# Kernel tuning notes

Hardware: AMD Instinct MI355X
Metric: run time of the kernel (lower is better)

The kernel has to match this reference:

```python
import jax, jax.numpy as jnp
import numpy as np

B, C, H, D, HID = 1024, 64, 64, 256, 256

def setup_inputs() -> dict:
    key = jax.random.key(0)
    k1, k2, k3, k4, k5, k6, k7, k8 = jax.random.split(key, 8)
    candidate_news_vector = jax.random.normal(k1, (B, C, D), dtype=jnp.float32)
    clicked_news_vector = jax.random.normal(k2, (B, H, D), dtype=jnp.float32)
    mask_cand = jax.random.randint(k3, (B, C), 0, 2).astype(bool).at[:, 0].set(True)
    mask_hist = jax.random.randint(k4, (B, H), 0, 2).astype(bool).at[:, 0].set(True)
    # nn.Linear default init: U(-1/sqrt(fan_in), 1/sqrt(fan_in))
    s1 = 1.0 / np.sqrt(2 * D)
    s2 = 1.0 / np.sqrt(HID)
    W1 = jax.random.uniform(k5, (HID, 2 * D), minval=-s1, maxval=s1, dtype=jnp.float32)
    b1 = jax.random.uniform(k6, (HID,), minval=-s1, maxval=s1, dtype=jnp.float32)
    W2 = jax.random.uniform(k7, (1, HID), minval=-s2, maxval=s2, dtype=jnp.float32)
    b2 = jax.random.uniform(k8, (1,), minval=-s2, maxval=s2, dtype=jnp.float32)
    return {"candidate_news_vector": candidate_news_vector,
            "clicked_news_vector": clicked_news_vector,
            "mask_cand": mask_cand, "mask_hist": mask_hist,
            "W1": W1, "b1": b1, "W2": W2, "b2": b2}

def reference(candidate_news_vector, clicked_news_vector, mask_cand, mask_hist, W1, b1, W2, b2):
    d = candidate_news_vector.shape[-1]
    w2 = W2[0]                                  # [HID]
    # Two stacked Linears with no nonlinearity collapse exactly:
    # score = (W2 @ W1_c) . cand + (W2 @ W1_h) . hist + (W2 @ b1 + b2)
    v_c = W1[:, :d].T @ w2                      # [D]
    v_h = W1[:, d:].T @ w2                      # [D]
    bias = jnp.dot(w2, b1) + b2[0]
    scores = (jnp.einsum('bcd,d->bc', candidate_news_vector, v_c)[:, :, None]
              + jnp.einsum('bhd,d->bh', clicked_news_vector, v_h)[:, None, :]
              + bias)                           # [B, C, H]
    neg = jnp.finfo(scores.dtype).min
    scores = jnp.where(mask_hist[:, None, :], scores, neg)
    weights = jax.nn.softmax(scores, axis=-1)   # [B, C, H]
    weights = jnp.where(mask_cand[:, :, None], weights, 0.0)
    user_vector = jnp.einsum('bch,bhd->bcd', weights, clicked_news_vector)
    return user_vector
```

## Files before the change

kernel.cpp:

```cpp
#include <hip/hip_runtime.h>
#include <math.h>

#define NB 1024
#define NC 64
#define NH 64
#define ND 256
#define NHID 256

__device__ __forceinline__ bool read_mask(const void* m, int idx, int mode) {
  if (mode == 2) return ((const float*)m)[idx] != 0.0f;
  if (mode == 1) return ((const unsigned char*)m)[idx] != 0;
  return ((const int*)m)[idx] != 0;
}

__global__ __launch_bounds__(1024) void precompute_kernel(
    const float* __restrict__ W1, const float* __restrict__ W2,
    const unsigned int* __restrict__ mask_cand,
    const unsigned int* __restrict__ mask_hist,
    float* __restrict__ ws)
{
  __shared__ float w2_lds[NHID];
  __shared__ float partial[4][ND];
  int t = threadIdx.x;
  if (t < NHID) w2_lds[t] = W2[t];
  __syncthreads();
  int d = t & (ND - 1);
  int g = t >> 8;
  float acc = 0.f;
  #pragma unroll 8
  for (int j = g * 64; j < g * 64 + 64; ++j)
    acc = fmaf(W1[(size_t)j * (2 * ND) + ND + d], w2_lds[j], acc);
  partial[g][d] = acc;
  __syncthreads();
  if (t < ND)
    ws[t] = partial[0][t] + partial[1][t] + partial[2][t] + partial[3][t];
  if (t == 0) {
    int sawf = 0; unsigned int big = 0;
    for (int i = 0; i < 32; ++i) {
      unsigned int a = mask_hist[i], b = mask_cand[i];
      if (a == 0x3f800000u || b == 0x3f800000u) sawf = 1;
      if ((a > 1u && a != 0x3f800000u) || (b > 1u && b != 0x3f800000u)) big = 1;
    }
    ((int*)ws)[ND] = sawf ? 2 : (big ? 1 : 0);
  }
}

__global__ __launch_bounds__(256) void user_encoder_kernel(
    const float* __restrict__ hist,
    const void* __restrict__ mask_cand_v,
    const void* __restrict__ mask_hist_v,
    const float* __restrict__ ws,
    float* __restrict__ out)
{
  const int b = blockIdx.x;
  const int t = threadIdx.x;
  const int wave = t >> 6;
  const int lane = t & 63;

  __shared__ float s_lds[NH];
  __shared__ float w_lds[NH];
  __shared__ float4 part[4][64];
  __shared__ float4 uv_lds[64];

  const int mode = ((const int*)ws)[ND];
  const float* hb = hist + (size_t)b * NH * ND;

  float4 xs[16];
  #pragma unroll
  for (int hh = 0; hh < 16; ++hh)
    xs[hh] = reinterpret_cast<const float4*>(hb + (size_t)(wave * 16 + hh) * ND)[lane];

  const float4 vh4 = reinterpret_cast<const float4*>(ws)[lane];
  #pragma unroll
  for (int hh = 0; hh < 16; ++hh) {
    float4 x = xs[hh];
    float p = fmaf(x.x, vh4.x, fmaf(x.y, vh4.y, fmaf(x.z, vh4.z, x.w * vh4.w)));
    #pragma unroll
    for (int off = 32; off; off >>= 1) p += __shfl_xor(p, off);
    if (lane == 0) {
      int h = wave * 16 + hh;
      bool mh = read_mask(mask_hist_v, b * NH + h, mode);
      s_lds[h] = mh ? p : -3.0e38f;
    }
  }
  __syncthreads();

  if (wave == 0) {
    float s = s_lds[lane];
    float m = s;
    #pragma unroll
    for (int off = 32; off; off >>= 1) m = fmaxf(m, __shfl_xor(m, off));
    float e = expf(s - m);
    float sum = e;
    #pragma unroll
    for (int off = 32; off; off >>= 1) sum += __shfl_xor(sum, off);
    w_lds[lane] = e / sum;
  }
  __syncthreads();

  float4 acc = {0.f, 0.f, 0.f, 0.f};
  #pragma unroll
  for (int hh = 0; hh < 16; ++hh) {
    float wgt = w_lds[wave * 16 + hh];
    float4 x = xs[hh];
    acc.x = fmaf(wgt, x.x, acc.x);
    acc.y = fmaf(wgt, x.y, acc.y);
    acc.z = fmaf(wgt, x.z, acc.z);
    acc.w = fmaf(wgt, x.w, acc.w);
  }
  part[wave][lane] = acc;
  __syncthreads();
  if (t < 64) {
    float4 a = part[0][t], b4 = part[1][t], c4 = part[2][t], d4 = part[3][t];
    float4 s4;
    s4.x = a.x + b4.x + c4.x + d4.x;
    s4.y = a.y + b4.y + c4.y + d4.y;
    s4.z = a.z + b4.z + c4.z + d4.z;
    s4.w = a.w + b4.w + c4.w + d4.w;
    uv_lds[t] = s4;
  }
  __syncthreads();

  float4* ob = reinterpret_cast<float4*>(out + (size_t)b * NC * ND);
  const float4 val = uv_lds[lane];
  const float4 zero = {0.f, 0.f, 0.f, 0.f};
  #pragma unroll
  for (int k = 0; k < 16; ++k) {
    int c = k * 4 + wave;
    bool mc = read_mask(mask_cand_v, b * NC + c, mode);
    ob[k * 256 + t] = mc ? val : zero;
  }
}

extern "C" void kernel_launch(void* const* d_in, const int* in_sizes, int n_in,
                              void* d_out, int out_size, void* d_ws, size_t ws_size,
                              hipStream_t stream) {
  (void)in_sizes; (void)n_in; (void)out_size; (void)ws_size;
  const float* hist = (const float*)d_in[1];
  const void*  mask_cand = d_in[2];
  const void*  mask_hist = d_in[3];
  const float* W1 = (const float*)d_in[4];
  const float* W2 = (const float*)d_in[6];
  float* ws = (float*)d_ws;
  float* out = (float*)d_out;

  precompute_kernel<<<1, 1024, 0, stream>>>(
      W1, W2, (const unsigned int*)mask_cand, (const unsigned int*)mask_hist, ws);
  user_encoder_kernel<<<NB, 256, 0, stream>>>(hist, mask_cand, mask_hist, ws, out);
}
```

Baseline: 45.45 us.

## Parallelize W1 reduction across blocks and widen main kernel to 512 threads

```diff
diff --git a/kernel.cpp b/kernel.cpp
--- a/kernel.cpp
+++ b/kernel.cpp
@@ -7,13 +7,57 @@
 #define ND 256
 #define NHID 256
 
+typedef float f4 __attribute__((ext_vector_type(4)));
+
+#define WS_PART_OFF 1024
+
 __device__ __forceinline__ bool read_mask(const void* m, int idx, int mode) {
   if (mode == 2) return ((const float*)m)[idx] != 0.0f;
   if (mode == 1) return ((const unsigned char*)m)[idx] != 0;
   return ((const int*)m)[idx] != 0;
 }
 
-__global__ __launch_bounds__(1024) void precompute_kernel(
+__device__ __forceinline__ void detect_mode(const unsigned int* mask_cand,
+                                            const unsigned int* mask_hist,
+                                            int* dst) {
+  int sawf = 0; unsigned int big = 0;
+  for (int i = 0; i < 32; ++i) {
+    unsigned int a = mask_hist[i], b = mask_cand[i];
+    if (a == 0x3f800000u || b == 0x3f800000u) sawf = 1;
+    if ((a > 1u && a != 0x3f800000u) || (b > 1u && b != 0x3f800000u)) big = 1;
+  }
+  *dst = sawf ? 2 : (big ? 1 : 0);
+}
+
+__global__ __launch_bounds__(256) void precompute_p1(
+    const float* __restrict__ W1, const float* __restrict__ W2,
+    float* __restrict__ ws)
+{
+  const int g = blockIdx.x;
+  const int d = threadIdx.x;
+  float acc = 0.f;
+  #pragma unroll
+  for (int jj = 0; jj < 4; ++jj) {
+    int j = g * 4 + jj;
+    acc = fmaf(W1[(size_t)j * (2 * ND) + ND + d], W2[j], acc);
+  }
+  ws[WS_PART_OFF + g * ND + d] = acc;
+}
+
+__global__ __launch_bounds__(256) void precompute_p2(
+    const unsigned int* __restrict__ mask_cand,
+    const unsigned int* __restrict__ mask_hist,
+    float* __restrict__ ws)
+{
+  const int d = threadIdx.x;
+  float acc = 0.f;
+  #pragma unroll 8
+  for (int g = 0; g < 64; ++g) acc += ws[WS_PART_OFF + g * ND + d];
+  ws[d] = acc;
+  if (d == 0) detect_mode(mask_cand, mask_hist, (int*)ws + ND);
+}
+
+__global__ __launch_bounds__(1024) void precompute_fallback(
     const float* __restrict__ W1, const float* __restrict__ W2,
     const unsigned int* __restrict__ mask_cand,
     const unsigned int* __restrict__ mask_hist,
@@ -34,18 +78,10 @@
   __syncthreads();
   if (t < ND)
     ws[t] = partial[0][t] + partial[1][t] + partial[2][t] + partial[3][t];
-  if (t == 0) {
-    int sawf = 0; unsigned int big = 0;
-    for (int i = 0; i < 32; ++i) {
-      unsigned int a = mask_hist[i], b = mask_cand[i];
-      if (a == 0x3f800000u || b == 0x3f800000u) sawf = 1;
-      if ((a > 1u && a != 0x3f800000u) || (b > 1u && b != 0x3f800000u)) big = 1;
-    }
-    ((int*)ws)[ND] = sawf ? 2 : (big ? 1 : 0);
-  }
+  if (t == 0) detect_mode(mask_cand, mask_hist, (int*)ws + ND);
 }
 
-__global__ __launch_bounds__(256) void user_encoder_kernel(
+__global__ __launch_bounds__(512, 8) void user_encoder_kernel(
     const float* __restrict__ hist,
     const void* __restrict__ mask_cand_v,
     const void* __restrict__ mask_hist_v,
@@ -54,38 +90,33 @@
 {
   const int b = blockIdx.x;
   const int t = threadIdx.x;
-  const int wave = t >> 6;
   const int lane = t & 63;
+  const int w = t >> 6;
 
   __shared__ float s_lds[NH];
-  __shared__ float w_lds[NH];
-  __shared__ float4 part[4][64];
-  __shared__ float4 uv_lds[64];
+  __shared__ float4 part[8][64];
 
   const int mode = ((const int*)ws)[ND];
-  const float* hb = hist + (size_t)b * NH * ND;
+  const float4* hb4 = reinterpret_cast<const float4*>(hist + (size_t)b * NH * ND);
+  const float4* vh4p = reinterpret_cast<const float4*>(ws);
 
-  float4 xs[16];
-  #pragma unroll
-  for (int hh = 0; hh < 16; ++hh)
-    xs[hh] = reinterpret_cast<const float4*>(hb + (size_t)(wave * 16 + hh) * ND)[lane];
-
-  const float4 vh4 = reinterpret_cast<const float4*>(ws)[lane];
-  #pragma unroll
-  for (int hh = 0; hh < 16; ++hh) {
-    float4 x = xs[hh];
-    float p = fmaf(x.x, vh4.x, fmaf(x.y, vh4.y, fmaf(x.z, vh4.z, x.w * vh4.w)));
+  {
+    const int r = t >> 3, cg = t & 7;
+    float p = 0.f;
     #pragma unroll
-    for (int off = 32; off; off >>= 1) p += __shfl_xor(p, off);
-    if (lane == 0) {
-      int h = wave * 16 + hh;
-      bool mh = read_mask(mask_hist_v, b * NH + h, mode);
-      s_lds[h] = mh ? p : -3.0e38f;
+    for (int i = 0; i < 8; ++i) {
+      float4 x = hb4[r * 64 + i * 8 + cg];
+      float4 v = vh4p[i * 8 + cg];
+      p = fmaf(x.x, v.x, fmaf(x.y, v.y, fmaf(x.z, v.z, fmaf(x.w, v.w, p))));
     }
+    p += __shfl_xor(p, 1); p += __shfl_xor(p, 2); p += __shfl_xor(p, 4);
+    if (cg == 0)
+      s_lds[r] = read_mask(mask_hist_v, b * NH + r, mode) ? p : -3.0e38f;
   }
   __syncthreads();
 
-  if (wave == 0) {
+  float wval;
+  {
     float s = s_lds[lane];
     float m = s;
     #pragma unroll
@@ -94,48 +125,46 @@
     float sum = e;
     #pragma unroll
     for (int off = 32; off; off >>= 1) sum += __shfl_xor(sum, off);
-    w_lds[lane] = e / sum;
+    wval = e / sum;
+  }
+
+  {
+    float4 acc = {0.f, 0.f, 0.f, 0.f};
+    #pragma unroll
+    for (int j = 0; j < 8; ++j) {
+      float wj = __shfl(wval, (w << 3) | j);
+      float4 x = hb4[((w << 3) | j) * 64 + lane];
+      acc.x = fmaf(wj, x.x, acc.x);
+      acc.y = fmaf(wj, x.y, acc.y);
+      acc.z = fmaf(wj, x.z, acc.z);
+      acc.w = fmaf(wj, x.w, acc.w);
+    }
+    part[w][lane] = acc;
   }
   __syncthreads();
 
-  float4 acc = {0.f, 0.f, 0.f, 0.f};
-  #pragma unroll
-  for (int hh = 0; hh < 16; ++hh) {
-    float wgt = w_lds[wave * 16 + hh];
-    float4 x = xs[hh];
-    acc.x = fmaf(wgt, x.x, acc.x);
-    acc.y = fmaf(wgt, x.y, acc.y);
-    acc.z = fmaf(wgt, x.z, acc.z);
-    acc.w = fmaf(wgt, x.w, acc.w);
-  }
-  part[wave][lane] = acc;
-  __syncthreads();
-  if (t < 64) {
-    float4 a = part[0][t], b4 = part[1][t], c4 = part[2][t], d4 = part[3][t];
-    float4 s4;
-    s4.x = a.x + b4.x + c4.x + d4.x;
-    s4.y = a.y + b4.y + c4.y + d4.y;
-    s4.z = a.z + b4.z + c4.z + d4.z;
-    s4.w = a.w + b4.w + c4.w + d4.w;
-    uv_lds[t] = s4;
-  }
-  __syncthreads();
-
-  float4* ob = reinterpret_cast<float4*>(out + (size_t)b * NC * ND);
-  const float4 val = uv_lds[lane];
-  const float4 zero = {0.f, 0.f, 0.f, 0.f};
-  #pragma unroll
-  for (int k = 0; k < 16; ++k) {
-    int c = k * 4 + wave;
-    bool mc = read_mask(mask_cand_v, b * NC + c, mode);
-    ob[k * 256 + t] = mc ? val : zero;
+  {
+    float4 uv = part[0][lane];
+    #pragma unroll
+    for (int g = 1; g < 8; ++g) {
+      float4 q = part[g][lane];
+      uv.x += q.x; uv.y += q.y; uv.z += q.z; uv.w += q.w;
+    }
+    float4* ob4 = reinterpret_cast<float4*>(out + (size_t)b * NC * ND);
+    #pragma unroll
+    for (int k = 0; k < 8; ++k) {
+      int c = w + k * 8;
+      bool mc = read_mask(mask_cand_v, b * NC + c, mode);
+      f4 val = mc ? (f4){uv.x, uv.y, uv.z, uv.w} : (f4){0.f, 0.f, 0.f, 0.f};
+      __builtin_nontemporal_store(val, reinterpret_cast<f4*>(&ob4[c * 64 + lane]));
+    }
   }
 }
 
 extern "C" void kernel_launch(void* const* d_in, const int* in_sizes, int n_in,
                               void* d_out, int out_size, void* d_ws, size_t ws_size,
                               hipStream_t stream) {
-  (void)in_sizes; (void)n_in; (void)out_size; (void)ws_size;
+  (void)in_sizes; (void)n_in; (void)out_size;
   const float* hist = (const float*)d_in[1];
   const void*  mask_cand = d_in[2];
   const void*  mask_hist = d_in[3];
@@ -144,7 +173,13 @@
   float* ws = (float*)d_ws;
   float* out = (float*)d_out;
 
-  precompute_kernel<<<1, 1024, 0, stream>>>(
-      W1, W2, (const unsigned int*)mask_cand, (const unsigned int*)mask_hist, ws);
-  user_encoder_kernel<<<NB, 256, 0, stream>>>(hist, mask_cand, mask_hist, ws, out);
+  if (ws_size >= (size_t)(WS_PART_OFF + 64 * ND) * sizeof(float)) {
+    precompute_p1<<<64, 256, 0, stream>>>(W1, W2, ws);
+    precompute_p2<<<1, 256, 0, stream>>>(
+        (const unsigned int*)mask_cand, (const unsigned int*)mask_hist, ws);
+  } else {
+    precompute_fallback<<<1, 1024, 0, stream>>>(
+        W1, W2, (const unsigned int*)mask_cand, (const unsigned int*)mask_hist, ws);
+  }
+  user_encoder_kernel<<<NB, 512, 0, stream>>>(hist, mask_cand, mask_hist, ws, out);
 }
```

Result: faster. 43.58 us (-4.1%).
